# Kernel tuning notes

Measured on AMD Instinct MI355X. Metric: run time of the kernel, lower is better.

## Reference

```python
import jax, jax.numpy as jnp
import numpy as np

N = 100000
E = 1600000
NODE_DIM = 64
H = 128
NUM_LAYERS = 3
NUM_CLASSES = 6
NUM_GRAPHS = 512
LN_EPS = 1e-5


def setup_inputs() -> dict:
    key = jax.random.key(0)
    ks = jax.random.split(key, 16)
    s = 0.05
    x = jax.random.normal(ks[0], (N, NODE_DIM), jnp.float32)
    edge_index = jax.random.randint(ks[1], (2, E), 0, N, dtype=jnp.int64)
    batch = jnp.sort(jax.random.randint(ks[2], (N,), 0, NUM_GRAPHS, dtype=jnp.int64))
    return {
        "x": x,
        "edge_index": edge_index,
        "batch": batch,
        "proj_w": jax.random.normal(ks[3], (NODE_DIM, H), jnp.float32) * s,
        "proj_b": jnp.zeros((H,), jnp.float32),
        "lin_l_w": jax.random.normal(ks[4], (NUM_LAYERS, H, H), jnp.float32) * s,
        "lin_l_b": jnp.zeros((NUM_LAYERS, H), jnp.float32),
        "lin_r_w": jax.random.normal(ks[5], (NUM_LAYERS, H, H), jnp.float32) * s,
        "ln_g": jnp.ones((NUM_LAYERS, H), jnp.float32),
        "ln_b": jnp.zeros((NUM_LAYERS, H), jnp.float32),
        "gate_w1": jax.random.normal(ks[6], (H, H // 2), jnp.float32) * s,
        "gate_b1": jnp.zeros((H // 2,), jnp.float32),
        "gate_w2": jax.random.normal(ks[7], (H // 2, 1), jnp.float32) * s,
        "gate_b2": jnp.zeros((1,), jnp.float32),
        "cls_w1": jax.random.normal(ks[8], (H, H // 2), jnp.float32) * s,
        "cls_b1": jnp.zeros((H // 2,), jnp.float32),
        "cls_w2": jax.random.normal(ks[9], (H // 2, NUM_CLASSES), jnp.float32) * s,
        "cls_b2": jnp.zeros((NUM_CLASSES,), jnp.float32),
    }


def _layer_norm(x, g, b):
    mu = jnp.mean(x, axis=-1, keepdims=True)
    var = jnp.mean(jnp.square(x - mu), axis=-1, keepdims=True)
    return (x - mu) * jax.lax.rsqrt(var + LN_EPS) * g + b


def _sage_mean_aggr(x, src, dst):
    # mean of source node features grouped by destination node
    summed = jax.ops.segment_sum(x[src], dst, num_segments=N)  # [N,H]
    deg = jax.ops.segment_sum(jnp.ones((E,), x.dtype), dst, num_segments=N)
    return summed / jnp.maximum(deg, 1.0)[:, None]


def reference(x, edge_index, batch, proj_w, proj_b, lin_l_w, lin_l_b, lin_r_w,
              ln_g, ln_b, gate_w1, gate_b1, gate_w2, gate_b2,
              cls_w1, cls_b1, cls_w2, cls_b2):
    src, dst = edge_index[0], edge_index[1]
    h = jax.nn.relu(x @ proj_w + proj_b)  # [N,H]
    for l in range(NUM_LAYERS):
        r = h
        aggr = _sage_mean_aggr(h, src, dst)
        # PyG SAGEConv: lin_l(aggregated) + lin_r(self), bias only in lin_l
        h = aggr @ lin_l_w[l] + lin_l_b[l] + h @ lin_r_w[l]
        h = _layer_norm(h, ln_g[l], ln_b[l])
        h = jax.nn.elu(h)
        h = h + r  # dropout is identity in eval mode
    # GlobalAttention pooling: segment softmax over nodes per graph
    gate = (jax.nn.relu(h @ gate_w1 + gate_b1) @ gate_w2 + gate_b2)[:, 0]  # [N]
    gmax = jax.ops.segment_max(gate, batch, num_segments=NUM_GRAPHS)
    eg = jnp.exp(gate - gmax[batch])
    denom = jax.ops.segment_sum(eg, batch, num_segments=NUM_GRAPHS)
    alpha = eg / denom[batch]  # [N]
    pooled = jax.ops.segment_sum(h * alpha[:, None], batch, num_segments=NUM_GRAPHS)  # [G,H]
    out = jax.nn.relu(pooled @ cls_w1 + cls_b1) @ cls_w2 + cls_b2  # [G,C]
    return out
```

## Files before the change

kernel.cpp:

```cpp
#include <hip/hip_runtime.h>
#include <hip/hip_fp16.h>
#include <math.h>

#define N_NODES   100000
#define N_EDGES   1600000
#define NDIM      64
#define H         128
#define NUM_LAYERS 3
#define NUM_CLASSES 6
#define NUM_GRAPHS 512
#define LN_EPS    1e-5f
#define NBKT      391
#define SCAP      5376
#define BPAD      136

typedef _Float16 f16x8 __attribute__((ext_vector_type(8)));
typedef float    f32x4 __attribute__((ext_vector_type(4)));

__device__ __forceinline__ int idx_at(const int* raw, int is64, int i) {
    return is64 ? raw[2 * (long long)i] : raw[i];
}
__device__ __forceinline__ int lower_bound(const int* a, int n, int v) {
    int lo = 0, hi = n;
    while (lo < hi) { int m = (lo + hi) >> 1; if (a[m] < v) lo = m + 1; else hi = m; }
    return lo;
}

__global__ void k_detect(const int* eraw, const int* braw, int* flags) {
    if (threadIdx.x == 0 && blockIdx.x == 0) {
        int e64 = 1;
        for (int i = 1; i < 128; i += 2) if (eraw[i] != 0) { e64 = 0; break; }
        flags[0] = e64;
        flags[1] = (braw[N_NODES - 1] == 0) ? 1 : 0;
    }
}

__global__ void k_init(int* bcnt) {
    int i = blockIdx.x * blockDim.x + threadIdx.x;
    if (i < 512) bcnt[i] = 0;
}

__global__ void k_conv_batch(const int* braw, const int* flags, int* batch32) {
    int i = blockIdx.x * blockDim.x + threadIdx.x;
    if (i < N_NODES) batch32[i] = idx_at(braw, flags[1], i);
}

__global__ __launch_bounds__(256) void k_bhist(const int* eraw, const int* flags, int* bcnt) {
    __shared__ int c[512];
    int tid = threadIdx.x;
    for (int i = tid; i < 512; i += 256) c[i] = 0;
    __syncthreads();
    int f = flags[0];
    int stride = gridDim.x * 256;
    for (int e = blockIdx.x * 256 + tid; e < N_EDGES; e += stride) {
        int d = idx_at(eraw, f, N_EDGES + e);
        atomicAdd(&c[d >> 8], 1);
    }
    __syncthreads();
    for (int i = tid; i < 512; i += 256) if (c[i]) atomicAdd(&bcnt[i], c[i]);
}

__global__ void k_bscan(const int* bcnt, int* boff, int* bcursor) {
    __shared__ int sh[512];
    int tid = threadIdx.x;
    int v = bcnt[tid];
    sh[tid] = v;
    __syncthreads();
    for (int off = 1; off < 512; off <<= 1) {
        int u = (tid >= off) ? sh[tid - off] : 0;
        __syncthreads();
        sh[tid] += u;
        __syncthreads();
    }
    int excl = sh[tid] - v;
    boff[tid] = excl;
    bcursor[tid] = excl;
    if (tid == 511) boff[512] = sh[511];
}

#define EPB 4096
__global__ __launch_bounds__(256) void k_bucket(const int* eraw, const int* flags,
                                                int* bcursor, unsigned int* br) {
    __shared__ int cnt[512];
    __shared__ int lcur[512];
    int tid = threadIdx.x;
    int f = flags[0];
    int base = blockIdx.x * EPB;
    int se[16], de[16];
#pragma unroll
    for (int j = 0; j < 16; ++j) {
        int e = base + j * 256 + tid;
        if (e < N_EDGES) {
            se[j] = idx_at(eraw, f, e);
            de[j] = idx_at(eraw, f, N_EDGES + e);
        } else de[j] = -1;
    }
    for (int i = tid; i < 512; i += 256) cnt[i] = 0;
    __syncthreads();
#pragma unroll
    for (int j = 0; j < 16; ++j)
        if (de[j] >= 0) atomicAdd(&cnt[de[j] >> 8], 1);
    __syncthreads();
    for (int i = tid; i < 512; i += 256)
        lcur[i] = cnt[i] ? atomicAdd(&bcursor[i], cnt[i]) : 0;
    __syncthreads();
#pragma unroll
    for (int j = 0; j < 16; ++j)
        if (de[j] >= 0) {
            int pos = atomicAdd(&lcur[de[j] >> 8], 1);
            br[pos] = ((unsigned int)(de[j] & 255) << 24) | (unsigned int)se[j];
        }
}

__global__ __launch_bounds__(256) void k_bdeg(const unsigned int* br, const int* boff, int* deg) {
    __shared__ int d256[256];
    int b = blockIdx.x;
    int tid = threadIdx.x;
    d256[tid] = 0;
    __syncthreads();
    int lo = boff[b], hi = boff[b + 1];
    for (int i = lo + tid; i < hi; i += 256)
        atomicAdd(&d256[br[i] >> 24], 1);
    __syncthreads();
    int node = (b << 8) + tid;
    if (node < N_NODES) deg[node] = d256[tid];
}

__global__ void k_scan1(const int* deg, int* rowptr, int* bsums) {
    __shared__ int sh[256];
    int tid = threadIdx.x;
    int i0 = blockIdx.x * 512 + tid * 2;
    int a = (i0 < N_NODES) ? deg[i0] : 0;
    int b = (i0 + 1 < N_NODES) ? deg[i0 + 1] : 0;
    int ts = a + b;
    sh[tid] = ts;
    __syncthreads();
    for (int off = 1; off < 256; off <<= 1) {
        int v = (tid >= off) ? sh[tid - off] : 0;
        __syncthreads();
        sh[tid] += v;
        __syncthreads();
    }
    int excl = sh[tid] - ts;
    if (i0 < N_NODES) rowptr[i0] = excl;
    if (i0 + 1 < N_NODES) rowptr[i0 + 1] = excl + a;
    if (tid == 255) bsums[blockIdx.x] = sh[255];
}

__global__ void k_scan2(int* bsums, int nb) {
    __shared__ int sh[256];
    int tid = threadIdx.x;
    int v = (tid < nb) ? bsums[tid] : 0;
    sh[tid] = v;
    __syncthreads();
    for (int off = 1; off < 256; off <<= 1) {
        int u = (tid >= off) ? sh[tid - off] : 0;
        __syncthreads();
        sh[tid] += u;
        __syncthreads();
    }
    if (tid < nb) bsums[tid] = sh[tid] - v;
}

__global__ void k_scan3(int* rowptr, const int* bsums, int* cursor) {
    int i = blockIdx.x * blockDim.x + threadIdx.x;
    if (i < N_NODES) {
        int r = rowptr[i] + bsums[i >> 9];
        rowptr[i] = r;
        cursor[i] = r;
    }
    if (i == 0) rowptr[N_NODES] = N_EDGES;
}

__global__ __launch_bounds__(256) void k_scatter2(const unsigned int* br, const int* boff,
                                                  const int* rowptr, int* cursor, int* col) {
    __shared__ int lcur[256];
    __shared__ int cbuf[SCAP];
    int b = blockIdx.x;
    int tid = threadIdx.x;
    int lo = boff[b], hi = boff[b + 1];
    int wsize = hi - lo;
    int node = (b << 8) + tid;
    lcur[tid] = rowptr[node < N_NODES ? node : N_NODES] - lo;
    __syncthreads();
    if (wsize <= SCAP) {
        for (int i = lo + tid; i < hi; i += 256) {
            unsigned int r = br[i];
            int p = atomicAdd(&lcur[r >> 24], 1);
            cbuf[p] = (int)(r & 0xFFFFFF);
        }
        __syncthreads();
        for (int j = tid; j < wsize; j += 256) col[lo + j] = cbuf[j] << 8;
    } else {
        for (int i = lo + tid; i < hi; i += 256) {
            unsigned int r = br[i];
            int d = (b << 8) + (int)(r >> 24);
            int p = atomicAdd(&cursor[d], 1);
            col[p] = (int)(r & 0xFFFFFF) << 8;
        }
    }
}

__global__ void k_prepw(const float* __restrict__ lin_l_w, const float* __restrict__ lin_r_w,
                        const float* __restrict__ gate_w1,
                        __half* __restrict__ W16t, __half* __restrict__ W16g) {
    int i = blockIdx.x * 256 + threadIdx.x;
    if (i < NUM_LAYERS * 128 * 256) {
        int l = i >> 15;
        int rem = i & 32767;
        int n = rem >> 8;
        int k = rem & 255;
        float v = (k < 128) ? lin_l_w[(size_t)l * 16384 + k * 128 + n]
                            : lin_r_w[(size_t)l * 16384 + (k - 128) * 128 + n];
        W16t[(size_t)l * 32768 + n * 256 + k] = __float2half(v);
    } else if (i < NUM_LAYERS * 128 * 256 + 64 * 128) {
        int idx = i - NUM_LAYERS * 128 * 256;
        int n = idx >> 7;
        int k = idx & 127;
        W16g[n * 128 + k] = __float2half(gate_w1[k * 64 + n]);
    }
}

__global__ __launch_bounds__(256) void k_gemm_proj(const float* __restrict__ A,
                                                   const float* __restrict__ W,
                                                   const float* __restrict__ bias,
                                                   __half* __restrict__ C16,
                                                   int nrows, int K) {
    __shared__ float As_t[32][68];
    __shared__ float Ws[32 * 128];
    int tid = threadIdx.x;
    int row0 = blockIdx.x * 64;
    int tr = tid >> 4;
    int tc = tid & 15;
    int c0 = tc * 8;
    float acc[4][8];
#pragma unroll
    for (int i = 0; i < 4; ++i)
#pragma unroll
        for (int j = 0; j < 8; ++j) acc[i][j] = 0.f;

    for (int kc = 0; kc < K; kc += 32) {
        __syncthreads();
#pragma unroll
        for (int it = 0; it < 2; ++it) {
            int idx = tid + it * 256;
            int r = idx >> 3, c4 = idx & 7;
            int gr = row0 + r;
            float4 v = make_float4(0.f, 0.f, 0.f, 0.f);
            if (gr < nrows) v = *(const float4*)(A + (size_t)gr * K + kc + c4 * 4);
            As_t[c4 * 4 + 0][r] = v.x;
            As_t[c4 * 4 + 1][r] = v.y;
            As_t[c4 * 4 + 2][r] = v.z;
            As_t[c4 * 4 + 3][r] = v.w;
        }
#pragma unroll
        for (int it = 0; it < 4; ++it) {
            int idx = tid + it * 256;
            int r = idx >> 5, c4 = idx & 31;
            *(float4*)(&Ws[r * 128 + c4 * 4]) = *(const float4*)(W + (size_t)(kc + r) * 128 + c4 * 4);
        }
        __syncthreads();
#pragma unroll
        for (int k = 0; k < 32; ++k) {
            float4 a4 = *(const float4*)(&As_t[k][tr * 4]);
            float a[4] = {a4.x, a4.y, a4.z, a4.w};
            float4 w0 = *(const float4*)(&Ws[k * 128 + c0]);
            float4 w1 = *(const float4*)(&Ws[k * 128 + c0 + 4]);
            float w[8] = {w0.x, w0.y, w0.z, w0.w, w1.x, w1.y, w1.z, w1.w};
#pragma unroll
            for (int i = 0; i < 4; ++i)
#pragma unroll
                for (int j = 0; j < 8; ++j) acc[i][j] += a[i] * w[j];
        }
    }
    float bv[8];
#pragma unroll
    for (int j = 0; j < 8; ++j) bv[j] = bias[c0 + j];
#pragma unroll
    for (int i = 0; i < 4; ++i) {
        int gr = row0 + tr * 4 + i;
        if (gr < nrows) {
            float o[8];
#pragma unroll
            for (int j = 0; j < 8; ++j) o[j] = fmaxf(acc[i][j] + bv[j], 0.f);
            __half2 p[4];
#pragma unroll
            for (int j = 0; j < 8; j += 2) p[j / 2] = __floats2half2_rn(o[j], o[j + 1]);
            *(float4*)(C16 + (size_t)gr * 128 + c0) = *(float4*)p;
        }
    }
}

__global__ __launch_bounds__(256) void k_gate_mfma(const __half* __restrict__ h16,
                                                   const __half* __restrict__ W16g,
                                                   const float* __restrict__ b1,
                                                   const float* __restrict__ w2,
                                                   const float* __restrict__ b2,
                                                   float* __restrict__ gate) {
    __shared__ __half Bs[64 * BPAD];
    int tid = threadIdx.x;
    int wave = tid >> 6, lane = tid & 63;
    int s = lane & 15, quad = lane >> 4;
    int row0 = blockIdx.x * 64 + wave * 16;
    int arow = row0 + s;
    if (arow >= N_NODES) arow = N_NODES - 1;

#pragma unroll
    for (int it = 0; it < 4; ++it) {
        int idx = tid + it * 256;
        int n = idx >> 4, ch = idx & 15;
        *(float4*)(&Bs[n * BPAD + ch * 8]) = *(const float4*)(W16g + (size_t)n * 128 + ch * 8);
    }
    __syncthreads();

    f32x4 acc[4];
#pragma unroll
    for (int c = 0; c < 4; ++c) acc[c] = (f32x4){0.f, 0.f, 0.f, 0.f};

    const __half* aptr = h16 + (size_t)arow * H;
#pragma unroll
    for (int kc = 0; kc < 128; kc += 32) {
        f16x8 afrag = *(const f16x8*)(aptr + kc + quad * 8);
#pragma unroll
        for (int c = 0; c < 4; ++c) {
            f16x8 bfrag = *(const f16x8*)(&Bs[(c * 16 + s) * BPAD + kc + quad * 8]);
            acc[c] = __builtin_amdgcn_mfma_f32_16x16x32_f16(afrag, bfrag, acc[c], 0, 0, 0);
        }
    }
    float part[4] = {0.f, 0.f, 0.f, 0.f};
#pragma unroll
    for (int c = 0; c < 4; ++c) {
        float bv = b1[c * 16 + s];
        float wv = w2[c * 16 + s];
#pragma unroll
        for (int i = 0; i < 4; ++i)
            part[i] += fmaxf(acc[c][i] + bv, 0.f) * wv;
    }
#pragma unroll
    for (int off = 1; off < 16; off <<= 1) {
#pragma unroll
        for (int i = 0; i < 4; ++i) part[i] += __shfl_xor(part[i], off);
    }
    if (s == 0) {
        float b2v = b2[0];
#pragma unroll
        for (int i = 0; i < 4; ++i) {
            int r = row0 + quad * 4 + i;
            if (r < N_NODES) gate[r] = part[i] + b2v;
        }
    }
}

__global__ __launch_bounds__(64) void k_softmax_g(float* __restrict__ gate,
                                                  const int* __restrict__ batch32,
                                                  float* __restrict__ gsum) {
    int g = blockIdx.x;
    int lane = threadIdx.x;
    int n0 = lower_bound(batch32, N_NODES, g);
    int n1 = lower_bound(batch32, N_NODES, g + 1);
    float m = -INFINITY;
    for (int n = n0 + lane; n < n1; n += 64) m = fmaxf(m, gate[n]);
#pragma unroll
    for (int off = 32; off >= 1; off >>= 1) m = fmaxf(m, __shfl_xor(m, off));
    float s = 0.f;
    for (int n = n0 + lane; n < n1; n += 64) {
        float e = expf(gate[n] - m);
        gate[n] = e;
        s += e;
    }
#pragma unroll
    for (int off = 32; off >= 1; off >>= 1) s += __shfl_xor(s, off);
    if (lane == 0) gsum[g] = s;
}

__global__ __launch_bounds__(256) void k_pool_g(const __half* __restrict__ h16,
                                                const float* __restrict__ eg,
                                                const float* __restrict__ gsum,
                                                const int* __restrict__ batch32,
                                                float* __restrict__ pooled) {
    __shared__ float sacc[256];
    int g = blockIdx.x;
    int tid = threadIdx.x;
    int c = tid & 127;
    int p = tid >> 7;
    int n0 = lower_bound(batch32, N_NODES, g);
    int n1 = lower_bound(batch32, N_NODES, g + 1);
    float acc = 0.f;
    for (int n = n0 + p; n < n1; n += 2)
        acc += eg[n] * __half2float(h16[(size_t)n * H + c]);
    sacc[tid] = acc;
    __syncthreads();
    if (tid < 128) {
        float s = gsum[g];
        float v = sacc[tid] + sacc[tid + 128];
        pooled[(size_t)g * H + tid] = (n1 > n0) ? v / s : 0.f;
    }
}

__global__ __launch_bounds__(256) void k_layer_mfma(const __half* __restrict__ t16,
                                                    __half* __restrict__ h16,
                                                    const __half* __restrict__ W16t,
                                                    const float* __restrict__ bl,
                                                    const float* __restrict__ g,
                                                    const float* __restrict__ bb) {
    __shared__ __half Bs[128 * BPAD];
    int tid = threadIdx.x;
    int wave = tid >> 6, lane = tid & 63;
    int s = lane & 15, quad = lane >> 4;
    int row0 = blockIdx.x * 64;
    int wrow0 = row0 + wave * 16;
    int arow = wrow0 + s;
    if (arow >= N_NODES) arow = N_NODES - 1;

    f32x4 acc[8];
#pragma unroll
    for (int c = 0; c < 8; ++c) acc[c] = (f32x4){0.f, 0.f, 0.f, 0.f};

#pragma unroll
    for (int ph = 0; ph < 2; ++ph) {
        __syncthreads();
#pragma unroll
        for (int it = 0; it < 8; ++it) {
            int idx = tid + it * 256;
            int n = idx >> 4, ch = idx & 15;
            *(float4*)(&Bs[n * BPAD + ch * 8]) =
                *(const float4*)(W16t + (size_t)n * 256 + ph * 128 + ch * 8);
        }
        __syncthreads();
        const __half* aptr = (ph ? h16 : t16) + (size_t)arow * H;
#pragma unroll
        for (int kk = 0; kk < 128; kk += 32) {
            f16x8 afrag = *(const f16x8*)(aptr + kk + quad * 8);
#pragma unroll
            for (int c = 0; c < 8; ++c) {
                f16x8 bfrag = *(const f16x8*)(&Bs[(c * 16 + s) * BPAD + kk + quad * 8]);
                acc[c] = __builtin_amdgcn_mfma_f32_16x16x32_f16(afrag, bfrag, acc[c], 0, 0, 0);
            }
        }
    }

    float y[8][4];
    float sm[4] = {0.f, 0.f, 0.f, 0.f}, sq[4] = {0.f, 0.f, 0.f, 0.f};
#pragma unroll
    for (int c = 0; c < 8; ++c) {
        float bv = bl[c * 16 + s];
#pragma unroll
        for (int i = 0; i < 4; ++i) {
            float v = acc[c][i] + bv;
            y[c][i] = v;
            sm[i] += v;
            sq[i] += v * v;
        }
    }
#pragma unroll
    for (int off = 1; off < 16; off <<= 1) {
#pragma unroll
        for (int i = 0; i < 4; ++i) {
            sm[i] += __shfl_xor(sm[i], off);
            sq[i] += __shfl_xor(sq[i], off);
        }
    }
    float mean[4], rstd[4];
#pragma unroll
    for (int i = 0; i < 4; ++i) {
        mean[i] = sm[i] * (1.0f / H);
        float var = sq[i] * (1.0f / H) - mean[i] * mean[i];
        rstd[i] = rsqrtf(var + LN_EPS);
    }
    float gv[8], bbv[8];
#pragma unroll
    for (int c = 0; c < 8; ++c) { gv[c] = g[c * 16 + s]; bbv[c] = bb[c * 16 + s]; }

    __syncthreads();
#pragma unroll
    for (int i = 0; i < 4; ++i) {
        int lr = wave * 16 + quad * 4 + i;
#pragma unroll
        for (int c = 0; c < 8; ++c) {
            float yv = (y[c][i] - mean[i]) * rstd[i] * gv[c] + bbv[c];
            yv = yv > 0.f ? yv : expf(yv) - 1.f;
            Bs[lr * BPAD + c * 16 + s] = __float2half(yv);
        }
    }
    __syncthreads();
#pragma unroll
    for (int it = 0; it < 4; ++it) {
        int idx = tid + it * 256;
        int r = idx >> 4, ch = idx & 15;
        int grow = row0 + r;
        if (grow < N_NODES) {
            float4 sv = *(float4*)(&Bs[r * BPAD + ch * 8]);
            float4 hv = *(const float4*)(h16 + (size_t)grow * H + ch * 8);
            __half2* pa = (__half2*)&sv;
            const __half2* pb = (const __half2*)&hv;
#pragma unroll
            for (int j = 0; j < 4; ++j) {
                float2 fa = __half22float2(pa[j]);
                float2 fb = __half22float2(pb[j]);
                pa[j] = __floats2half2_rn(fa.x + fb.x, fa.y + fb.y);
            }
            *(float4*)(h16 + (size_t)grow * H + ch * 8) = sv;
        }
    }
}

__global__ __launch_bounds__(256) void k_aggr(const __half* __restrict__ h16,
                                              const int* __restrict__ rowptr,
                                              const int* __restrict__ col,
                                              __half* __restrict__ t16) {
    int lane = threadIdx.x & 63;
    int node = blockIdx.x * 4 + (threadIdx.x >> 6);
    if (node >= N_NODES) return;
    int li = lane & 31;
    int pg = lane >> 5;
    int e0 = rowptr[node], e1 = rowptr[node + 1];
    const char* hbase = (const char*)h16 + li * 8;
    __half2 z = __floats2half2_rn(0.f, 0.f);
    __half2 a0 = z, a1 = z, b0 = z, b1 = z, c0 = z, c1 = z, d0 = z, d1 = z;
    int e = e0;
    for (; e + 7 < e1; e += 8) {
        float2 rA = *(const float2*)(hbase + col[e + pg]);
        float2 rB = *(const float2*)(hbase + col[e + 2 + pg]);
        float2 rC = *(const float2*)(hbase + col[e + 4 + pg]);
        float2 rD = *(const float2*)(hbase + col[e + 6 + pg]);
        const __half2* hA = (const __half2*)&rA;
        const __half2* hB = (const __half2*)&rB;
        const __half2* hC = (const __half2*)&rC;
        const __half2* hD = (const __half2*)&rD;
        a0 = __hadd2(a0, hA[0]); a1 = __hadd2(a1, hA[1]);
        b0 = __hadd2(b0, hB[0]); b1 = __hadd2(b1, hB[1]);
        c0 = __hadd2(c0, hC[0]); c1 = __hadd2(c1, hC[1]);
        d0 = __hadd2(d0, hD[0]); d1 = __hadd2(d1, hD[1]);
    }
    for (; e + 3 < e1; e += 4) {
        float2 rA = *(const float2*)(hbase + col[e + pg]);
        float2 rB = *(const float2*)(hbase + col[e + 2 + pg]);
        const __half2* hA = (const __half2*)&rA;
        const __half2* hB = (const __half2*)&rB;
        a0 = __hadd2(a0, hA[0]); a1 = __hadd2(a1, hA[1]);
        b0 = __hadd2(b0, hB[0]); b1 = __hadd2(b1, hB[1]);
    }
    for (; e + 1 < e1; e += 2) {
        float2 rA = *(const float2*)(hbase + col[e + pg]);
        const __half2* hA = (const __half2*)&rA;
        a0 = __hadd2(a0, hA[0]); a1 = __hadd2(a1, hA[1]);
    }
    if (e < e1 && pg == 0) {
        float2 rA = *(const float2*)(hbase + col[e]);
        const __half2* hA = (const __half2*)&rA;
        a0 = __hadd2(a0, hA[0]); a1 = __hadd2(a1, hA[1]);
    }
    float2 fa0 = __half22float2(a0), fb0 = __half22float2(b0);
    float2 fc0 = __half22float2(c0), fd0 = __half22float2(d0);
    float2 fa1 = __half22float2(a1), fb1 = __half22float2(b1);
    float2 fc1 = __half22float2(c1), fd1 = __half22float2(d1);
    float s0 = fa0.x + fb0.x + fc0.x + fd0.x;
    float s1 = fa0.y + fb0.y + fc0.y + fd0.y;
    float s2 = fa1.x + fb1.x + fc1.x + fd1.x;
    float s3 = fa1.y + fb1.y + fc1.y + fd1.y;
    s0 += __shfl_xor(s0, 32);
    s1 += __shfl_xor(s1, 32);
    s2 += __shfl_xor(s2, 32);
    s3 += __shfl_xor(s3, 32);
    if (pg == 0) {
        int d = e1 - e0;
        float inv = 1.0f / (float)(d > 1 ? d : 1);
        __half2 h01 = __floats2half2_rn(s0 * inv, s1 * inv);
        __half2 h23 = __floats2half2_rn(s2 * inv, s3 * inv);
        float2 o;
        ((__half2*)&o)[0] = h01;
        ((__half2*)&o)[1] = h23;
        *(float2*)(t16 + (size_t)node * H + li * 4) = o;
    }
}

__global__ __launch_bounds__(64) void k_cls(const float* __restrict__ pooled,
                                            const float* __restrict__ w1,
                                            const float* __restrict__ b1,
                                            const float* __restrict__ w2,
                                            const float* __restrict__ b2,
                                            float* __restrict__ out) {
    __shared__ float sp[64];
    int g = blockIdx.x;
    int lane = threadIdx.x;
    float r0 = pooled[(size_t)g * H + lane];
    float r1 = pooled[(size_t)g * H + 64 + lane];
    float acc = b1[lane];
#pragma unroll 16
    for (int k = 0; k < 64; ++k) acc += __shfl(r0, k) * w1[k * 64 + lane];
#pragma unroll 16
    for (int k = 0; k < 64; ++k) acc += __shfl(r1, k) * w1[(64 + k) * 64 + lane];
    sp[lane] = fmaxf(acc, 0.f);
    __syncthreads();
    if (lane < NUM_CLASSES) {
        float o = b2[lane];
        for (int c = 0; c < 64; ++c) o += sp[c] * w2[c * NUM_CLASSES + lane];
        out[g * NUM_CLASSES + lane] = o;
    }
}

extern "C" void kernel_launch(void* const* d_in, const int* in_sizes, int n_in,
                              void* d_out, int out_size, void* d_ws, size_t ws_size,
                              hipStream_t stream) {
    const float* x       = (const float*)d_in[0];
    const int*   eraw    = (const int*)d_in[1];
    const int*   braw    = (const int*)d_in[2];
    const float* proj_w  = (const float*)d_in[3];
    const float* proj_b  = (const float*)d_in[4];
    const float* lin_l_w = (const float*)d_in[5];
    const float* lin_l_b = (const float*)d_in[6];
    const float* lin_r_w = (const float*)d_in[7];
    const float* ln_g    = (const float*)d_in[8];
    const float* ln_b    = (const float*)d_in[9];
    const float* gate_w1 = (const float*)d_in[10];
    const float* gate_b1 = (const float*)d_in[11];
    const float* gate_w2 = (const float*)d_in[12];
    const float* gate_b2 = (const float*)d_in[13];
    const float* cls_w1  = (const float*)d_in[14];
    const float* cls_b1  = (const float*)d_in[15];
    const float* cls_w2  = (const float*)d_in[16];
    const float* cls_b2  = (const float*)d_in[17];
    float* out = (float*)d_out;

    __half* h16    = (__half*)d_ws;
    __half* t16    = h16 + (size_t)N_NODES * H;
    float*  gate   = (float*)(t16 + (size_t)N_NODES * H);
    float*  gsum   = gate + N_NODES;
    float*  pooled = gsum + NUM_GRAPHS;
    __half* W16t   = (__half*)(pooled + NUM_GRAPHS * H);
    __half* W16g   = W16t + (size_t)NUM_LAYERS * 32768;
    int* flags     = (int*)(W16g + 64 * 128);
    int* col       = flags + 4;
    int* batch32   = col + N_EDGES;
    int* deg       = batch32 + N_NODES;
    int* rowptr    = deg + N_NODES;
    int* cursor    = rowptr + N_NODES + 1;
    int* bsums     = cursor + N_NODES;
    int* bcnt      = bsums + 256;
    int* boff      = bcnt + 512;
    int* bcursor   = boff + 513;
    unsigned int* br = (unsigned int*)(bcursor + 512);

    const int nbN = (N_NODES + 255) / 256;
    const int nbE4 = (N_EDGES + EPB - 1) / EPB;
    const int nbS = (N_NODES + 511) / 512;
    const int nbW = (N_NODES + 3) / 4;
    const int nbG = (N_NODES + 63) / 64;
    const int nbP = (NUM_LAYERS * 128 * 256 + 64 * 128 + 255) / 256;

    k_detect<<<1, 1, 0, stream>>>(eraw, braw, flags);
    k_init<<<2, 256, 0, stream>>>(bcnt);
    k_conv_batch<<<nbN, 256, 0, stream>>>(braw, flags, batch32);
    k_bhist<<<512, 256, 0, stream>>>(eraw, flags, bcnt);
    k_bscan<<<1, 512, 0, stream>>>(bcnt, boff, bcursor);
    k_bucket<<<nbE4, 256, 0, stream>>>(eraw, flags, bcursor, br);
    k_bdeg<<<NBKT, 256, 0, stream>>>(br, boff, deg);
    k_scan1<<<nbS, 256, 0, stream>>>(deg, rowptr, bsums);
    k_scan2<<<1, 256, 0, stream>>>(bsums, nbS);
    k_scan3<<<nbN, 256, 0, stream>>>(rowptr, bsums, cursor);
    k_scatter2<<<NBKT, 256, 0, stream>>>(br, boff, rowptr, cursor, col);
    k_prepw<<<nbP, 256, 0, stream>>>(lin_l_w, lin_r_w, gate_w1, W16t, W16g);

    k_gemm_proj<<<nbG, 256, 0, stream>>>(x, proj_w, proj_b, h16, N_NODES, NDIM);

    for (int l = 0; l < NUM_LAYERS; ++l) {
        const float* bl  = lin_l_b + (size_t)l * H;
        const float* gl  = ln_g + (size_t)l * H;
        const float* blb = ln_b + (size_t)l * H;
        k_aggr<<<nbW, 256, 0, stream>>>(h16, rowptr, col, t16);
        k_layer_mfma<<<nbG, 256, 0, stream>>>(t16, h16, W16t + (size_t)l * 32768, bl, gl, blb);
    }

    k_gate_mfma<<<nbG, 256, 0, stream>>>(h16, W16g, gate_b1, gate_w2, gate_b2, gate);
    k_softmax_g<<<NUM_GRAPHS, 64, 0, stream>>>(gate, batch32, gsum);
    k_pool_g<<<NUM_GRAPHS, 256, 0, stream>>>(h16, gate, gsum, batch32, pooled);
    k_cls<<<NUM_GRAPHS, 64, 0, stream>>>(pooled, cls_w1, cls_b1, cls_w2, cls_b2, out);
}
```

Baseline: 508.6 us.

## Fuse mean aggregation into the SAGE layer MFMA kernel with ping-pong buffers

Merges the per-layer neighbour mean-aggregation kernel into the MFMA linear+LayerNorm+ELU+residual kernel. Each block gathers and averages its 64 nodes' neighbour rows into shared memory, then uses them directly as the A operand, so the aggregated intermediate is no longer written to and read back from global memory. Layers now read from one h buffer and write to another, avoiding in-place hazards now that neighbours are read in the same kernel. In exchange, the gather runs with only 64 nodes per block, one wave per 16 nodes processed serially, and weights are staged in four smaller K chunks, which may reduce latency hiding for the irregular gathers.

```diff
diff --git a/kernel.cpp b/kernel.cpp
--- a/kernel.cpp
+++ b/kernel.cpp
@@ -13,6 +13,8 @@
 #define NBKT      391
 #define SCAP      5376
 #define BPAD      136
+#define APAD      136
+#define BPAD2     72
 
 typedef _Float16 f16x8 __attribute__((ext_vector_type(8)));
 typedef float    f32x4 __attribute__((ext_vector_type(4)));
@@ -291,6 +293,183 @@
     }
 }
 
+__global__ __launch_bounds__(256) void k_aggr_layer(const __half* __restrict__ hin,
+                                                    __half* __restrict__ hout,
+                                                    const int* __restrict__ rowptr,
+                                                    const int* __restrict__ col,
+                                                    const __half* __restrict__ W16t,
+                                                    const float* __restrict__ bl,
+                                                    const float* __restrict__ g,
+                                                    const float* __restrict__ bb) {
+    __shared__ __half As[64 * APAD];
+    __shared__ __half Bs[128 * BPAD2];
+    int tid = threadIdx.x;
+    int wave = tid >> 6, lane = tid & 63;
+    int li = lane & 31, pg = lane >> 5;
+    int s = lane & 15, quad = lane >> 4;
+    int row0 = blockIdx.x * 64;
+
+    const char* hbase = (const char*)hin + li * 8;
+    for (int j = 0; j < 16; ++j) {
+        int node = row0 + wave * 16 + j;
+        int e0 = 0, e1 = 0;
+        if (node < N_NODES) { e0 = rowptr[node]; e1 = rowptr[node + 1]; }
+        __half2 z = __floats2half2_rn(0.f, 0.f);
+        __half2 a0 = z, a1 = z, b0 = z, b1 = z, c0 = z, c1 = z, d0 = z, d1 = z;
+        int e = e0;
+        for (; e + 7 < e1; e += 8) {
+            float2 rA = *(const float2*)(hbase + col[e + pg]);
+            float2 rB = *(const float2*)(hbase + col[e + 2 + pg]);
+            float2 rC = *(const float2*)(hbase + col[e + 4 + pg]);
+            float2 rD = *(const float2*)(hbase + col[e + 6 + pg]);
+            const __half2* hA = (const __half2*)&rA;
+            const __half2* hB = (const __half2*)&rB;
+            const __half2* hC = (const __half2*)&rC;
+            const __half2* hD = (const __half2*)&rD;
+            a0 = __hadd2(a0, hA[0]); a1 = __hadd2(a1, hA[1]);
+            b0 = __hadd2(b0, hB[0]); b1 = __hadd2(b1, hB[1]);
+            c0 = __hadd2(c0, hC[0]); c1 = __hadd2(c1, hC[1]);
+            d0 = __hadd2(d0, hD[0]); d1 = __hadd2(d1, hD[1]);
+        }
+        for (; e + 3 < e1; e += 4) {
+            float2 rA = *(const float2*)(hbase + col[e + pg]);
+            float2 rB = *(const float2*)(hbase + col[e + 2 + pg]);
+            const __half2* hA = (const __half2*)&rA;
+            const __half2* hB = (const __half2*)&rB;
+            a0 = __hadd2(a0, hA[0]); a1 = __hadd2(a1, hA[1]);
+            b0 = __hadd2(b0, hB[0]); b1 = __hadd2(b1, hB[1]);
+        }
+        for (; e + 1 < e1; e += 2) {
+            float2 rA = *(const float2*)(hbase + col[e + pg]);
+            const __half2* hA = (const __half2*)&rA;
+            a0 = __hadd2(a0, hA[0]); a1 = __hadd2(a1, hA[1]);
+        }
+        if (e < e1 && pg == 0) {
+            float2 rA = *(const float2*)(hbase + col[e]);
+            const __half2* hA = (const __half2*)&rA;
+            a0 = __hadd2(a0, hA[0]); a1 = __hadd2(a1, hA[1]);
+        }
+        float2 fa0 = __half22float2(a0), fb0 = __half22float2(b0);
+        float2 fc0 = __half22float2(c0), fd0 = __half22float2(d0);
+        float2 fa1 = __half22float2(a1), fb1 = __half22float2(b1);
+        float2 fc1 = __half22float2(c1), fd1 = __half22float2(d1);
+        float s0 = fa0.x + fb0.x + fc0.x + fd0.x;
+        float s1 = fa0.y + fb0.y + fc0.y + fd0.y;
+        float s2 = fa1.x + fb1.x + fc1.x + fd1.x;
+        float s3 = fa1.y + fb1.y + fc1.y + fd1.y;
+        s0 += __shfl_xor(s0, 32);
+        s1 += __shfl_xor(s1, 32);
+        s2 += __shfl_xor(s2, 32);
+        s3 += __shfl_xor(s3, 32);
+        if (pg == 0) {
+            int d = e1 - e0;
+            float inv = 1.0f / (float)(d > 1 ? d : 1);
+            __half2 h01 = __floats2half2_rn(s0 * inv, s1 * inv);
+            __half2 h23 = __floats2half2_rn(s2 * inv, s3 * inv);
+            float2 o;
+            ((__half2*)&o)[0] = h01;
+            ((__half2*)&o)[1] = h23;
+            *(float2*)(&As[(wave * 16 + j) * APAD + li * 4]) = o;
+        }
+    }
+
+    int arow = row0 + wave * 16 + s;
+    if (arow >= N_NODES) arow = N_NODES - 1;
+    f32x4 acc[8];
+#pragma unroll
+    for (int c = 0; c < 8; ++c) acc[c] = (f32x4){0.f, 0.f, 0.f, 0.f};
+
+#pragma unroll
+    for (int c4 = 0; c4 < 4; ++c4) {
+        __syncthreads();
+#pragma unroll
+        for (int it = 0; it < 4; ++it) {
+            int idx = tid + it * 256;
+            int n = idx >> 3, f4 = idx & 7;
+            *(float4*)(&Bs[n * BPAD2 + f4 * 8]) =
+                *(const float4*)(W16t + (size_t)n * 256 + c4 * 64 + f4 * 8);
+        }
+        __syncthreads();
+#pragma unroll
+        for (int kk = 0; kk < 64; kk += 32) {
+            f16x8 afrag;
+            if (c4 < 2)
+                afrag = *(const f16x8*)(&As[(wave * 16 + s) * APAD + c4 * 64 + kk + quad * 8]);
+            else
+                afrag = *(const f16x8*)(hin + (size_t)arow * H + (c4 - 2) * 64 + kk + quad * 8);
+#pragma unroll
+            for (int c = 0; c < 8; ++c) {
+                f16x8 bfrag = *(const f16x8*)(&Bs[(c * 16 + s) * BPAD2 + kk + quad * 8]);
+                acc[c] = __builtin_amdgcn_mfma_f32_16x16x32_f16(afrag, bfrag, acc[c], 0, 0, 0);
+            }
+        }
+    }
+
+    float y[8][4];
+    float sm[4] = {0.f, 0.f, 0.f, 0.f}, sq[4] = {0.f, 0.f, 0.f, 0.f};
+#pragma unroll
+    for (int c = 0; c < 8; ++c) {
+        float bv = bl[c * 16 + s];
+#pragma unroll
+        for (int i = 0; i < 4; ++i) {
+            float v = acc[c][i] + bv;
+            y[c][i] = v;
+            sm[i] += v;
+            sq[i] += v * v;
+        }
+    }
+#pragma unroll
+    for (int off = 1; off < 16; off <<= 1) {
+#pragma unroll
+        for (int i = 0; i < 4; ++i) {
+            sm[i] += __shfl_xor(sm[i], off);
+            sq[i] += __shfl_xor(sq[i], off);
+        }
+    }
+    float mean[4], rstd[4];
+#pragma unroll
+    for (int i = 0; i < 4; ++i) {
+        mean[i] = sm[i] * (1.0f / H);
+        float var = sq[i] * (1.0f / H) - mean[i] * mean[i];
+        rstd[i] = rsqrtf(var + LN_EPS);
+    }
+    float gv[8], bbv[8];
+#pragma unroll
+    for (int c = 0; c < 8; ++c) { gv[c] = g[c * 16 + s]; bbv[c] = bb[c * 16 + s]; }
+
+    __syncthreads();
+#pragma unroll
+    for (int i = 0; i < 4; ++i) {
+        int lr = wave * 16 + quad * 4 + i;
+#pragma unroll
+        for (int c = 0; c < 8; ++c) {
+            float yv = (y[c][i] - mean[i]) * rstd[i] * gv[c] + bbv[c];
+            yv = yv > 0.f ? yv : expf(yv) - 1.f;
+            As[lr * APAD + c * 16 + s] = __float2half(yv);
+        }
+    }
+    __syncthreads();
+#pragma unroll
+    for (int it = 0; it < 4; ++it) {
+        int idx = tid + it * 256;
+        int r = idx >> 4, ch = idx & 15;
+        int grow = row0 + r;
+        if (grow < N_NODES) {
+            float4 sv = *(float4*)(&As[r * APAD + ch * 8]);
+            float4 hv = *(const float4*)(hin + (size_t)grow * H + ch * 8);
+            __half2* pa = (__half2*)&sv;
+            const __half2* pb = (const __half2*)&hv;
+#pragma unroll
+            for (int j = 0; j < 4; ++j) {
+                float2 fa = __half22float2(pa[j]);
+                float2 fb = __half22float2(pb[j]);
+                pa[j] = __floats2half2_rn(fa.x + fb.x, fa.y + fb.y);
+            }
+            *(float4*)(hout + (size_t)grow * H + ch * 8) = sv;
+        }
+    }
+}
+
 __global__ __launch_bounds__(256) void k_gate_mfma(const __half* __restrict__ h16,
                                                    const __half* __restrict__ W16g,
                                                    const float* __restrict__ b1,
@@ -394,183 +573,6 @@
         float s = gsum[g];
         float v = sacc[tid] + sacc[tid + 128];
         pooled[(size_t)g * H + tid] = (n1 > n0) ? v / s : 0.f;
-    }
-}
-
-__global__ __launch_bounds__(256) void k_layer_mfma(const __half* __restrict__ t16,
-                                                    __half* __restrict__ h16,
-                                                    const __half* __restrict__ W16t,
-                                                    const float* __restrict__ bl,
-                                                    const float* __restrict__ g,
-                                                    const float* __restrict__ bb) {
-    __shared__ __half Bs[128 * BPAD];
-    int tid = threadIdx.x;
-    int wave = tid >> 6, lane = tid & 63;
-    int s = lane & 15, quad = lane >> 4;
-    int row0 = blockIdx.x * 64;
-    int wrow0 = row0 + wave * 16;
-    int arow = wrow0 + s;
-    if (arow >= N_NODES) arow = N_NODES - 1;
-
-    f32x4 acc[8];
-#pragma unroll
-    for (int c = 0; c < 8; ++c) acc[c] = (f32x4){0.f, 0.f, 0.f, 0.f};
-
-#pragma unroll
-    for (int ph = 0; ph < 2; ++ph) {
-        __syncthreads();
-#pragma unroll
-        for (int it = 0; it < 8; ++it) {
-            int idx = tid + it * 256;
-            int n = idx >> 4, ch = idx & 15;
-            *(float4*)(&Bs[n * BPAD + ch * 8]) =
-                *(const float4*)(W16t + (size_t)n * 256 + ph * 128 + ch * 8);
-        }
-        __syncthreads();
-        const __half* aptr = (ph ? h16 : t16) + (size_t)arow * H;
-#pragma unroll
-        for (int kk = 0; kk < 128; kk += 32) {
-            f16x8 afrag = *(const f16x8*)(aptr + kk + quad * 8);
-#pragma unroll
-            for (int c = 0; c < 8; ++c) {
-                f16x8 bfrag = *(const f16x8*)(&Bs[(c * 16 + s) * BPAD + kk + quad * 8]);
-                acc[c] = __builtin_amdgcn_mfma_f32_16x16x32_f16(afrag, bfrag, acc[c], 0, 0, 0);
-            }
-        }
-    }
-
-    float y[8][4];
-    float sm[4] = {0.f, 0.f, 0.f, 0.f}, sq[4] = {0.f, 0.f, 0.f, 0.f};
-#pragma unroll
-    for (int c = 0; c < 8; ++c) {
-        float bv = bl[c * 16 + s];
-#pragma unroll
-        for (int i = 0; i < 4; ++i) {
-            float v = acc[c][i] + bv;
-            y[c][i] = v;
-            sm[i] += v;
-            sq[i] += v * v;
-        }
-    }
-#pragma unroll
-    for (int off = 1; off < 16; off <<= 1) {
-#pragma unroll
-        for (int i = 0; i < 4; ++i) {
-            sm[i] += __shfl_xor(sm[i], off);
-            sq[i] += __shfl_xor(sq[i], off);
-        }
-    }
-    float mean[4], rstd[4];
-#pragma unroll
-    for (int i = 0; i < 4; ++i) {
-        mean[i] = sm[i] * (1.0f / H);
-        float var = sq[i] * (1.0f / H) - mean[i] * mean[i];
-        rstd[i] = rsqrtf(var + LN_EPS);
-    }
-    float gv[8], bbv[8];
-#pragma unroll
-    for (int c = 0; c < 8; ++c) { gv[c] = g[c * 16 + s]; bbv[c] = bb[c * 16 + s]; }
-
-    __syncthreads();
-#pragma unroll
-    for (int i = 0; i < 4; ++i) {
-        int lr = wave * 16 + quad * 4 + i;
-#pragma unroll
-        for (int c = 0; c < 8; ++c) {
-            float yv = (y[c][i] - mean[i]) * rstd[i] * gv[c] + bbv[c];
-            yv = yv > 0.f ? yv : expf(yv) - 1.f;
-            Bs[lr * BPAD + c * 16 + s] = __float2half(yv);
-        }
-    }
-    __syncthreads();
-#pragma unroll
-    for (int it = 0; it < 4; ++it) {
-        int idx = tid + it * 256;
-        int r = idx >> 4, ch = idx & 15;
-        int grow = row0 + r;
-        if (grow < N_NODES) {
-            float4 sv = *(float4*)(&Bs[r * BPAD + ch * 8]);
-            float4 hv = *(const float4*)(h16 + (size_t)grow * H + ch * 8);
-            __half2* pa = (__half2*)&sv;
-            const __half2* pb = (const __half2*)&hv;
-#pragma unroll
-            for (int j = 0; j < 4; ++j) {
-                float2 fa = __half22float2(pa[j]);
-                float2 fb = __half22float2(pb[j]);
-                pa[j] = __floats2half2_rn(fa.x + fb.x, fa.y + fb.y);
-            }
-            *(float4*)(h16 + (size_t)grow * H + ch * 8) = sv;
-        }
-    }
-}
-
-__global__ __launch_bounds__(256) void k_aggr(const __half* __restrict__ h16,
-                                              const int* __restrict__ rowptr,
-                                              const int* __restrict__ col,
-                                              __half* __restrict__ t16) {
-    int lane = threadIdx.x & 63;
-    int node = blockIdx.x * 4 + (threadIdx.x >> 6);
-    if (node >= N_NODES) return;
-    int li = lane & 31;
-    int pg = lane >> 5;
-    int e0 = rowptr[node], e1 = rowptr[node + 1];
-    const char* hbase = (const char*)h16 + li * 8;
-    __half2 z = __floats2half2_rn(0.f, 0.f);
-    __half2 a0 = z, a1 = z, b0 = z, b1 = z, c0 = z, c1 = z, d0 = z, d1 = z;
-    int e = e0;
-    for (; e + 7 < e1; e += 8) {
-        float2 rA = *(const float2*)(hbase + col[e + pg]);
-        float2 rB = *(const float2*)(hbase + col[e + 2 + pg]);
-        float2 rC = *(const float2*)(hbase + col[e + 4 + pg]);
-        float2 rD = *(const float2*)(hbase + col[e + 6 + pg]);
-        const __half2* hA = (const __half2*)&rA;
-        const __half2* hB = (const __half2*)&rB;
-        const __half2* hC = (const __half2*)&rC;
-        const __half2* hD = (const __half2*)&rD;
-        a0 = __hadd2(a0, hA[0]); a1 = __hadd2(a1, hA[1]);
-        b0 = __hadd2(b0, hB[0]); b1 = __hadd2(b1, hB[1]);
-        c0 = __hadd2(c0, hC[0]); c1 = __hadd2(c1, hC[1]);
-        d0 = __hadd2(d0, hD[0]); d1 = __hadd2(d1, hD[1]);
-    }
-    for (; e + 3 < e1; e += 4) {
-        float2 rA = *(const float2*)(hbase + col[e + pg]);
-        float2 rB = *(const float2*)(hbase + col[e + 2 + pg]);
-        const __half2* hA = (const __half2*)&rA;
-        const __half2* hB = (const __half2*)&rB;
-        a0 = __hadd2(a0, hA[0]); a1 = __hadd2(a1, hA[1]);
-        b0 = __hadd2(b0, hB[0]); b1 = __hadd2(b1, hB[1]);
-    }
-    for (; e + 1 < e1; e += 2) {
-        float2 rA = *(const float2*)(hbase + col[e + pg]);
-        const __half2* hA = (const __half2*)&rA;
-        a0 = __hadd2(a0, hA[0]); a1 = __hadd2(a1, hA[1]);
-    }
-    if (e < e1 && pg == 0) {
-        float2 rA = *(const float2*)(hbase + col[e]);
-        const __half2* hA = (const __half2*)&rA;
-        a0 = __hadd2(a0, hA[0]); a1 = __hadd2(a1, hA[1]);
-    }
-    float2 fa0 = __half22float2(a0), fb0 = __half22float2(b0);
-    float2 fc0 = __half22float2(c0), fd0 = __half22float2(d0);
-    float2 fa1 = __half22float2(a1), fb1 = __half22float2(b1);
-    float2 fc1 = __half22float2(c1), fd1 = __half22float2(d1);
-    float s0 = fa0.x + fb0.x + fc0.x + fd0.x;
-    float s1 = fa0.y + fb0.y + fc0.y + fd0.y;
-    float s2 = fa1.x + fb1.x + fc1.x + fd1.x;
-    float s3 = fa1.y + fb1.y + fc1.y + fd1.y;
-    s0 += __shfl_xor(s0, 32);
-    s1 += __shfl_xor(s1, 32);
-    s2 += __shfl_xor(s2, 32);
-    s3 += __shfl_xor(s3, 32);
-    if (pg == 0) {
-        int d = e1 - e0;
-        float inv = 1.0f / (float)(d > 1 ? d : 1);
-        __half2 h01 = __floats2half2_rn(s0 * inv, s1 * inv);
-        __half2 h23 = __floats2half2_rn(s2 * inv, s3 * inv);
-        float2 o;
-        ((__half2*)&o)[0] = h01;
-        ((__half2*)&o)[1] = h23;
-        *(float2*)(t16 + (size_t)node * H + li * 4) = o;
     }
 }
 
@@ -622,9 +624,9 @@
     const float* cls_b2  = (const float*)d_in[17];
     float* out = (float*)d_out;
 
-    __half* h16    = (__half*)d_ws;
-    __half* t16    = h16 + (size_t)N_NODES * H;
-    float*  gate   = (float*)(t16 + (size_t)N_NODES * H);
+    __half* hA     = (__half*)d_ws;
+    __half* hB     = hA + (size_t)N_NODES * H;
+    float*  gate   = (float*)(hB + (size_t)N_NODES * H);
     float*  gsum   = gate + N_NODES;
     float*  pooled = gsum + NUM_GRAPHS;
     __half* W16t   = (__half*)(pooled + NUM_GRAPHS * H);
@@ -644,7 +646,6 @@
     const int nbN = (N_NODES + 255) / 256;
     const int nbE4 = (N_EDGES + EPB - 1) / EPB;
     const int nbS = (N_NODES + 511) / 512;
-    const int nbW = (N_NODES + 3) / 4;
     const int nbG = (N_NODES + 63) / 64;
     const int nbP = (NUM_LAYERS * 128 * 256 + 64 * 128 + 255) / 256;
 
@@ -661,18 +662,22 @@
     k_scatter2<<<NBKT, 256, 0, stream>>>(br, boff, rowptr, cursor, col);
     k_prepw<<<nbP, 256, 0, stream>>>(lin_l_w, lin_r_w, gate_w1, W16t, W16g);
 
-    k_gemm_proj<<<nbG, 256, 0, stream>>>(x, proj_w, proj_b, h16, N_NODES, NDIM);
-
+    k_gemm_proj<<<nbG, 256, 0, stream>>>(x, proj_w, proj_b, hA, N_NODES, NDIM);
+
+    __half* hin = hA;
+    __half* hout = hB;
     for (int l = 0; l < NUM_LAYERS; ++l) {
         const float* bl  = lin_l_b + (size_t)l * H;
         const float* gl  = ln_g + (size_t)l * H;
         const float* blb = ln_b + (size_t)l * H;
-        k_aggr<<<nbW, 256, 0, stream>>>(h16, rowptr, col, t16);
-        k_layer_mfma<<<nbG, 256, 0, stream>>>(t16, h16, W16t + (size_t)l * 32768, bl, gl, blb);
-    }
-
-    k_gate_mfma<<<nbG, 256, 0, stream>>>(h16, W16g, gate_b1, gate_w2, gate_b2, gate);
+        k_aggr_layer<<<nbG, 256, 0, stream>>>(hin, hout, rowptr, col,
+                                              W16t + (size_t)l * 32768, bl, gl, blb);
+        __half* tmp = hin; hin = hout; hout = tmp;
+    }
+    __half* hfin = hin;
+
+    k_gate_mfma<<<nbG, 256, 0, stream>>>(hfin, W16g, gate_b1, gate_w2, gate_b2, gate);
     k_softmax_g<<<NUM_GRAPHS, 64, 0, stream>>>(gate, batch32, gsum);
-    k_pool_g<<<NUM_GRAPHS, 256, 0, stream>>>(h16, gate, gsum, batch32, pooled);
+    k_pool_g<<<NUM_GRAPHS, 256, 0, stream>>>(hfin, gate, gsum, batch32, pooled);
     k_cls<<<NUM_GRAPHS, 64, 0, stream>>>(pooled, cls_w1, cls_b1, cls_w2, cls_b2, out);
 }
```

Measured after the change: 729.0 us. +43.3%, slower.

## Fuse degree count, row-pointer scan and column scatter into one CSR kernel

Applied to the files above, without the earlier changes.

Merges the per-bucket degree histogram, the three-pass global prefix scan and the column scatter into a single kernel per 256-node bucket. Each bucket's row offsets come from the bucket base offset plus a local shared-memory scan, so the global scan passes and the global cursor array are no longer needed. This removes four kernel launches and the round trips through the deg, bsums and cursor arrays. In exchange each block does more shared-memory work and keeps the cbuf staging footprint.

```diff
diff --git a/kernel.cpp b/kernel.cpp
--- a/kernel.cpp
+++ b/kernel.cpp
@@ -112,81 +112,40 @@
         }
 }
 
-__global__ __launch_bounds__(256) void k_bdeg(const unsigned int* br, const int* boff, int* deg) {
+__global__ __launch_bounds__(256) void k_csr_tail(const unsigned int* br, const int* boff,
+                                                  int* rowptr, int* col) {
     __shared__ int d256[256];
+    __shared__ int sc[256];
+    __shared__ int cbuf[SCAP];
     int b = blockIdx.x;
     int tid = threadIdx.x;
+    int lo = boff[b], hi = boff[b + 1];
+    int wsize = hi - lo;
     d256[tid] = 0;
     __syncthreads();
-    int lo = boff[b], hi = boff[b + 1];
     for (int i = lo + tid; i < hi; i += 256)
         atomicAdd(&d256[br[i] >> 24], 1);
     __syncthreads();
+    int v = d256[tid];
+    sc[tid] = v;
+    __syncthreads();
+    for (int off = 1; off < 256; off <<= 1) {
+        int u = (tid >= off) ? sc[tid - off] : 0;
+        __syncthreads();
+        sc[tid] += u;
+        __syncthreads();
+    }
+    int excl = sc[tid] - v;
     int node = (b << 8) + tid;
-    if (node < N_NODES) deg[node] = d256[tid];
-}
-
-__global__ void k_scan1(const int* deg, int* rowptr, int* bsums) {
-    __shared__ int sh[256];
-    int tid = threadIdx.x;
-    int i0 = blockIdx.x * 512 + tid * 2;
-    int a = (i0 < N_NODES) ? deg[i0] : 0;
-    int b = (i0 + 1 < N_NODES) ? deg[i0 + 1] : 0;
-    int ts = a + b;
-    sh[tid] = ts;
-    __syncthreads();
-    for (int off = 1; off < 256; off <<= 1) {
-        int v = (tid >= off) ? sh[tid - off] : 0;
-        __syncthreads();
-        sh[tid] += v;
-        __syncthreads();
-    }
-    int excl = sh[tid] - ts;
-    if (i0 < N_NODES) rowptr[i0] = excl;
-    if (i0 + 1 < N_NODES) rowptr[i0 + 1] = excl + a;
-    if (tid == 255) bsums[blockIdx.x] = sh[255];
-}
-
-__global__ void k_scan2(int* bsums, int nb) {
-    __shared__ int sh[256];
-    int tid = threadIdx.x;
-    int v = (tid < nb) ? bsums[tid] : 0;
-    sh[tid] = v;
-    __syncthreads();
-    for (int off = 1; off < 256; off <<= 1) {
-        int u = (tid >= off) ? sh[tid - off] : 0;
-        __syncthreads();
-        sh[tid] += u;
-        __syncthreads();
-    }
-    if (tid < nb) bsums[tid] = sh[tid] - v;
-}
-
-__global__ void k_scan3(int* rowptr, const int* bsums, int* cursor) {
-    int i = blockIdx.x * blockDim.x + threadIdx.x;
-    if (i < N_NODES) {
-        int r = rowptr[i] + bsums[i >> 9];
-        rowptr[i] = r;
-        cursor[i] = r;
-    }
-    if (i == 0) rowptr[N_NODES] = N_EDGES;
-}
-
-__global__ __launch_bounds__(256) void k_scatter2(const unsigned int* br, const int* boff,
-                                                  const int* rowptr, int* cursor, int* col) {
-    __shared__ int lcur[256];
-    __shared__ int cbuf[SCAP];
-    int b = blockIdx.x;
-    int tid = threadIdx.x;
-    int lo = boff[b], hi = boff[b + 1];
-    int wsize = hi - lo;
-    int node = (b << 8) + tid;
-    lcur[tid] = rowptr[node < N_NODES ? node : N_NODES] - lo;
+    if (node < N_NODES) rowptr[node] = lo + excl;
+    if (b == NBKT - 1 && tid == 0) rowptr[N_NODES] = N_EDGES;
+    __syncthreads();
+    d256[tid] = excl;
     __syncthreads();
     if (wsize <= SCAP) {
         for (int i = lo + tid; i < hi; i += 256) {
             unsigned int r = br[i];
-            int p = atomicAdd(&lcur[r >> 24], 1);
+            int p = atomicAdd(&d256[r >> 24], 1);
             cbuf[p] = (int)(r & 0xFFFFFF);
         }
         __syncthreads();
@@ -194,9 +153,8 @@
     } else {
         for (int i = lo + tid; i < hi; i += 256) {
             unsigned int r = br[i];
-            int d = (b << 8) + (int)(r >> 24);
-            int p = atomicAdd(&cursor[d], 1);
-            col[p] = (int)(r & 0xFFFFFF) << 8;
+            int p = atomicAdd(&d256[r >> 24], 1);
+            col[lo + p] = (int)(r & 0xFFFFFF) << 8;
         }
     }
 }
@@ -632,18 +590,14 @@
     int* flags     = (int*)(W16g + 64 * 128);
     int* col       = flags + 4;
     int* batch32   = col + N_EDGES;
-    int* deg       = batch32 + N_NODES;
-    int* rowptr    = deg + N_NODES;
-    int* cursor    = rowptr + N_NODES + 1;
-    int* bsums     = cursor + N_NODES;
-    int* bcnt      = bsums + 256;
+    int* rowptr    = batch32 + N_NODES;
+    int* bcnt      = rowptr + N_NODES + 1;
     int* boff      = bcnt + 512;
     int* bcursor   = boff + 513;
     unsigned int* br = (unsigned int*)(bcursor + 512);
 
     const int nbN = (N_NODES + 255) / 256;
     const int nbE4 = (N_EDGES + EPB - 1) / EPB;
-    const int nbS = (N_NODES + 511) / 512;
     const int nbW = (N_NODES + 3) / 4;
     const int nbG = (N_NODES + 63) / 64;
     const int nbP = (NUM_LAYERS * 128 * 256 + 64 * 128 + 255) / 256;
@@ -654,11 +608,7 @@
     k_bhist<<<512, 256, 0, stream>>>(eraw, flags, bcnt);
     k_bscan<<<1, 512, 0, stream>>>(bcnt, boff, bcursor);
     k_bucket<<<nbE4, 256, 0, stream>>>(eraw, flags, bcursor, br);
-    k_bdeg<<<NBKT, 256, 0, stream>>>(br, boff, deg);
-    k_scan1<<<nbS, 256, 0, stream>>>(deg, rowptr, bsums);
-    k_scan2<<<1, 256, 0, stream>>>(bsums, nbS);
-    k_scan3<<<nbN, 256, 0, stream>>>(rowptr, bsums, cursor);
-    k_scatter2<<<NBKT, 256, 0, stream>>>(br, boff, rowptr, cursor, col);
+    k_csr_tail<<<NBKT, 256, 0, stream>>>(br, boff, rowptr, col);
     k_prepw<<<nbP, 256, 0, stream>>>(lin_l_w, lin_r_w, gate_w1, W16t, W16g);
 
     k_gemm_proj<<<nbG, 256, 0, stream>>>(x, proj_w, proj_b, h16, N_NODES, NDIM);
```

New measurement: 498.2 us. 1.02x faster.
